# Optimization experiments

Measured on AMD Instinct MI355X. Metric: run time of the kernel, lower is better.

Reference implementation:

```python
import jax, jax.numpy as jnp
import numpy as np

B, T, DIM = 8, 2048, 512
DM, EXPAND, NSTATE, HDIM, L = 128, 2, 16, 64, 2
DINNER = DM * EXPAND            # 256
NH = DINNER // HDIM             # 4 heads
CONVDIM = DINNER + 2 * NSTATE   # 288 (n_groups=1)
PROJ = DINNER + CONVDIM + NH    # 548
K = 4                           # conv kernel (HF default)
EPS = 1e-5


def setup_inputs() -> dict:
    key = jax.random.key(0)
    ks = jax.random.split(key, 8)
    s = 0.02
    return {
        "x": jax.random.normal(ks[0], (B, T, DIM), jnp.float32),
        "in_w": jax.random.normal(ks[1], (DIM, DM), jnp.float32) * s,
        "in_b": jnp.zeros((DM,), jnp.float32),
        "norm_w": jnp.ones((L, DM), jnp.float32),
        "inproj_w": jax.random.normal(ks[2], (L, DM, PROJ), jnp.float32) * s,
        "conv_w": jax.random.normal(ks[3], (L, CONVDIM, 1, K), jnp.float32) * 0.2,
        "conv_b": jnp.zeros((L, CONVDIM), jnp.float32),
        "A_log": jnp.log(jax.random.uniform(ks[4], (L, NH), jnp.float32, 1.0, 8.0)),
        "D": jnp.ones((L, NH), jnp.float32),
        "dt_bias": jnp.log(jnp.expm1(jax.random.uniform(ks[5], (L, NH), jnp.float32, 1e-3, 0.1))),
        "gnorm_w": jnp.ones((L, DINNER), jnp.float32),
        "outproj_w": jax.random.normal(ks[6], (L, DINNER, DM), jnp.float32) * s,
        "normf_w": jnp.ones((DM,), jnp.float32),
        "out_w": jax.random.normal(ks[7], (DM, DIM), jnp.float32) * s,
        "out_b": jnp.zeros((DIM,), jnp.float32),
    }


def _rmsnorm(x, w):
    var = jnp.mean(x * x, axis=-1, keepdims=True)
    return x * jax.lax.rsqrt(var + EPS) * w


def _gated_rmsnorm(y, gate, w):
    y = y * jax.nn.silu(gate)
    var = jnp.mean(y * y, axis=-1, keepdims=True)
    return y * jax.lax.rsqrt(var + EPS) * w


def _causal_conv(h, w, b):
    # h: [B,T,C] depthwise causal conv, kernel K, left pad K-1
    out = jax.lax.conv_general_dilated(
        h.swapaxes(1, 2), w, (1,), [(K - 1, 0)],
        feature_group_count=CONVDIM,
        dimension_numbers=("NCH", "OIH", "NCH"))
    return out.swapaxes(1, 2) + b


def _ssd(xs, dt, A, Bm, Cm, Dh):
    # selective state-space scan (math-equivalent to HF Mamba2 chunked SSD)
    # xs [B,T,H,P], dt [B,T,H], A [H], Bm/Cm [B,T,N], Dh [H]
    dA = jnp.exp(dt * A)  # [B,T,H]

    def step(state, inp):
        dA_t, dt_t, x_t, B_t, C_t = inp
        dBx = dt_t[:, :, None, None] * x_t[..., None] * B_t[:, None, None, :]
        state = state * dA_t[:, :, None, None] + dBx  # [B,H,P,N]
        y = jnp.einsum("bhpn,bn->bhp", state, C_t)
        return state, y

    init = jnp.zeros((xs.shape[0], NH, HDIM, NSTATE), xs.dtype)
    _, ys = jax.lax.scan(step, init, (dA.swapaxes(0, 1), dt.swapaxes(0, 1),
                                      xs.swapaxes(0, 1), Bm.swapaxes(0, 1), Cm.swapaxes(0, 1)))
    return ys.swapaxes(0, 1) + xs * Dh[None, None, :, None]


def reference(x, in_w, in_b, norm_w, inproj_w, conv_w, conv_b, A_log, D,
              dt_bias, gnorm_w, outproj_w, normf_w, out_w, out_b):
    h = x @ in_w + in_b  # [B,T,DM]
    for l in range(L):
        res = h
        hn = _rmsnorm(h, norm_w[l])
        proj = hn @ inproj_w[l]  # [B,T,PROJ]
        gate = proj[..., :DINNER]
        hBC = proj[..., DINNER:DINNER + CONVDIM]
        dt = proj[..., DINNER + CONVDIM:]
        hBC = jax.nn.silu(_causal_conv(hBC, conv_w[l], conv_b[l]))
        xs = hBC[..., :DINNER].reshape(B, T, NH, HDIM)
        Bm = hBC[..., DINNER:DINNER + NSTATE]
        Cm = hBC[..., DINNER + NSTATE:]
        A = -jnp.exp(A_log[l])
        dt = jax.nn.softplus(dt + dt_bias[l])  # time_step_limit=(0,inf): no clamp
        y = _ssd(xs, dt, A, Bm, Cm, D[l]).reshape(B, T, DINNER)
        y = _gated_rmsnorm(y, gate, gnorm_w[l])
        h = res + y @ outproj_w[l]
    h = _rmsnorm(h, normf_w)
    pooled = h.mean(axis=1)  # mean pool over T
    return pooled @ out_w + out_b
```

## Files before the change

kernel.cpp:

```cpp
#include <hip/hip_runtime.h>
#include <math.h>

typedef unsigned short ushort_t;
typedef unsigned int uint_t;

#define B_      8
#define T_      2048
#define DIMX    512
#define DM      128
#define DINNER  256
#define NSTATE  16
#define HDIM    64
#define NH      4
#define CONVDIM 288
#define PROJ    548
#define KCONV   4
#define LLAYERS 2
#define QCH     128
#define NC      (T_/QCH)
#define EPSF    1e-5f
#define MTOK    (B_*T_)

#define OFF_H      0u
#define OFF_Z      20119552u
#define OFF_DEC    21168128u
#define OFF_PART   21168640u
#define OFF_WTIN   23396864u
#define OFF_WTINP  23429632u
#define OFF_WTOUT  23503360u
#define OFF_PROJB  23600000u
#define OFF_DTRAW  28100000u
#define OFF_YB     30600000u

__device__ __forceinline__ ushort_t f2b(float f) {
    uint_t u = __builtin_bit_cast(uint_t, f);
    return (ushort_t)((u + 0x7FFFu + ((u >> 16) & 1u)) >> 16);
}
__device__ __forceinline__ float b2f(ushort_t b) {
    uint_t u = ((uint_t)b) << 16;
    return __builtin_bit_cast(float, u);
}
__device__ __forceinline__ float blo(uint_t u) { return b2f((ushort_t)(u & 0xffffu)); }
__device__ __forceinline__ float bhi(uint_t u) { return b2f((ushort_t)(u >> 16)); }

typedef short bf8 __attribute__((ext_vector_type(8)));
typedef float f4v __attribute__((ext_vector_type(4)));

__global__ __launch_bounds__(256) void k_wt_all(
    const float* __restrict__ in_w, const float* __restrict__ inproj_w,
    const float* __restrict__ outproj_w,
    ushort_t* __restrict__ wt_in, ushort_t* __restrict__ wt_inp,
    ushort_t* __restrict__ wt_out)
{
    __shared__ float tile[64][65];
    int idx = blockIdx.x;
    const float* W; ushort_t* Wt; int K, N, k0, n0;
    if (idx < 16) {
        W = in_w; Wt = wt_in; K = 512; N = 128;
        k0 = (idx & 7) * 64; n0 = (idx >> 3) * 64;
    } else if (idx < 52) {
        int r = idx - 16; int l = r / 18; r -= l * 18;
        W = inproj_w + l * 128 * PROJ; Wt = wt_inp + l * 576 * 128; K = 128; N = PROJ;
        k0 = (r & 1) * 64; n0 = (r >> 1) * 64;
    } else {
        int r = idx - 52; int l = r / 8; r -= l * 8;
        W = outproj_w + l * 256 * 128; Wt = wt_out + l * 128 * 256; K = 256; N = 128;
        k0 = (r & 3) * 64; n0 = (r >> 2) * 64;
    }
    const int tid = threadIdx.x;
#pragma unroll
    for (int it = 0; it < 16; ++it) {
        const int e = it * 256 + tid;
        const int kk = e >> 6, nn = e & 63;
        tile[kk][nn] = (n0 + nn < N) ? W[(k0 + kk) * N + (n0 + nn)] : 0.f;
    }
    __syncthreads();
#pragma unroll
    for (int it = 0; it < 16; ++it) {
        const int e = it * 256 + tid;
        const int nn = e >> 6, kk = e & 63;
        Wt[(n0 + nn) * K + k0 + kk] = f2b(tile[kk][nn]);
    }
}

template<int KTOT, int LDC, int NGUARD, int EPI, bool ABF16>
__global__ __launch_bounds__(256) void k_gemm(
    const void* __restrict__ Ap, const ushort_t* __restrict__ Bt,
    const float* __restrict__ aux, float* __restrict__ C)
{
    __shared__ ushort_t Als[64 * 136];
    __shared__ ushort_t Bls[64 * 136];
    const int m0 = blockIdx.x * 64, n0 = blockIdx.y * 64;
    const int tid = threadIdx.x;
    const int lane = tid & 63, w = tid >> 6;
    const int wm = (w >> 1) * 32, wn = (w & 1) * 32;
    const int r16 = lane & 15, q8 = (lane >> 4) * 8;

    f4v acc[2][2];
#pragma unroll
    for (int i = 0; i < 2; ++i)
#pragma unroll
        for (int j = 0; j < 2; ++j) acc[i][j] = (f4v)0.f;

    for (int kc = 0; kc < KTOT; kc += 128) {
        if constexpr (ABF16) {
            const ushort_t* A = (const ushort_t*)Ap;
#pragma unroll
            for (int i = 0; i < 4; ++i) {
                const int e = i * 2048 + tid * 8;
                const int r = e >> 7, c = e & 127;
                *(uint4*)&Als[r * 136 + c] = *(const uint4*)&A[(m0 + r) * KTOT + kc + c];
            }
        } else {
            const float* A = (const float*)Ap;
#pragma unroll
            for (int i = 0; i < 4; ++i) {
                const int e = i * 2048 + tid * 8;
                const int r = e >> 7, c = e & 127;
                const float4 f0 = *(const float4*)&A[(m0 + r) * KTOT + kc + c];
                const float4 f1 = *(const float4*)&A[(m0 + r) * KTOT + kc + c + 4];
                uint4 pk;
                pk.x = (uint_t)f2b(f0.x) | ((uint_t)f2b(f0.y) << 16);
                pk.y = (uint_t)f2b(f0.z) | ((uint_t)f2b(f0.w) << 16);
                pk.z = (uint_t)f2b(f1.x) | ((uint_t)f2b(f1.y) << 16);
                pk.w = (uint_t)f2b(f1.z) | ((uint_t)f2b(f1.w) << 16);
                *(uint4*)&Als[r * 136 + c] = pk;
            }
        }
#pragma unroll
        for (int i = 0; i < 4; ++i) {
            const int e = i * 2048 + tid * 8;
            const int r = e >> 7, c = e & 127;
            *(uint4*)&Bls[r * 136 + c] = *(const uint4*)&Bt[(n0 + r) * KTOT + kc + c];
        }
        __syncthreads();
#pragma unroll
        for (int kk = 0; kk < 128; kk += 32) {
            const bf8 a0 = *(const bf8*)&Als[(wm + r16) * 136 + kk + q8];
            const bf8 a1 = *(const bf8*)&Als[(wm + 16 + r16) * 136 + kk + q8];
            const bf8 b0 = *(const bf8*)&Bls[(wn + r16) * 136 + kk + q8];
            const bf8 b1 = *(const bf8*)&Bls[(wn + 16 + r16) * 136 + kk + q8];
            acc[0][0] = __builtin_amdgcn_mfma_f32_16x16x32_bf16(a0, b0, acc[0][0], 0, 0, 0);
            acc[0][1] = __builtin_amdgcn_mfma_f32_16x16x32_bf16(a0, b1, acc[0][1], 0, 0, 0);
            acc[1][0] = __builtin_amdgcn_mfma_f32_16x16x32_bf16(a1, b0, acc[1][0], 0, 0, 0);
            acc[1][1] = __builtin_amdgcn_mfma_f32_16x16x32_bf16(a1, b1, acc[1][1], 0, 0, 0);
        }
        __syncthreads();
    }
    const int q4 = (lane >> 4) * 4;
#pragma unroll
    for (int i = 0; i < 2; ++i)
#pragma unroll
        for (int j = 0; j < 2; ++j)
#pragma unroll
            for (int r = 0; r < 4; ++r) {
                const int grow = m0 + wm + i * 16 + q4 + r;
                const int gcol = n0 + wn + j * 16 + r16;
                if (NGUARD == 0 || gcol < NGUARD) {
                    float v = acc[i][j][r];
                    if (EPI == 1) v += aux[gcol];
                    if (EPI == 2) v += C[grow * LDC + gcol];
                    C[grow * LDC + gcol] = v;
                }
            }
}

__global__ __launch_bounds__(256) void k_gemm_rms(
    const float* __restrict__ h, const float* __restrict__ nw,
    const ushort_t* __restrict__ Bt, ushort_t* __restrict__ projb,
    float* __restrict__ dtraw)
{
    __shared__ ushort_t Als[64 * 136];
    __shared__ ushort_t Bls[64 * 136];
    const int m0 = blockIdx.x * 64;
    const int tid = threadIdx.x;
    const int lane = tid & 63, w = tid >> 6;
    const int wm = (w >> 1) * 32, wn = (w & 1) * 32;
    const int r16 = lane & 15, q8 = (lane >> 4) * 8;
    const int q4 = (lane >> 4) * 4;

#pragma unroll
    for (int i = 0; i < 4; ++i) {
        const int e = i * 2048 + tid * 8;
        const int r = e >> 7, c = e & 127;
        const float4 f0 = *(const float4*)&h[(m0 + r) * 128 + c];
        const float4 f1 = *(const float4*)&h[(m0 + r) * 128 + c + 4];
        float ss = f0.x * f0.x + f0.y * f0.y + f0.z * f0.z + f0.w * f0.w
                 + f1.x * f1.x + f1.y * f1.y + f1.z * f1.z + f1.w * f1.w;
#pragma unroll
        for (int off = 1; off < 16; off <<= 1) ss += __shfl_xor(ss, off);
        const float rs = rsqrtf(ss * (1.f / 128.f) + EPSF);
        const float4 w0 = *(const float4*)&nw[c];
        const float4 w1 = *(const float4*)&nw[c + 4];
        uint4 pk;
        pk.x = (uint_t)f2b(f0.x * rs * w0.x) | ((uint_t)f2b(f0.y * rs * w0.y) << 16);
        pk.y = (uint_t)f2b(f0.z * rs * w0.z) | ((uint_t)f2b(f0.w * rs * w0.w) << 16);
        pk.z = (uint_t)f2b(f1.x * rs * w1.x) | ((uint_t)f2b(f1.y * rs * w1.y) << 16);
        pk.w = (uint_t)f2b(f1.z * rs * w1.z) | ((uint_t)f2b(f1.w * rs * w1.w) << 16);
        *(uint4*)&Als[r * 136 + c] = pk;
    }

#pragma unroll
    for (int half = 0; half < 2; ++half) {
        const int n0 = blockIdx.y * 128 + half * 64;
        if (n0 >= 576) break;
#pragma unroll
        for (int i = 0; i < 4; ++i) {
            const int e = i * 2048 + tid * 8;
            const int r = e >> 7, c = e & 127;
            *(uint4*)&Bls[r * 136 + c] = *(const uint4*)&Bt[(n0 + r) * 128 + c];
        }
        __syncthreads();

        f4v acc[2][2];
#pragma unroll
        for (int i = 0; i < 2; ++i)
#pragma unroll
            for (int j = 0; j < 2; ++j) acc[i][j] = (f4v)0.f;
#pragma unroll
        for (int kk = 0; kk < 128; kk += 32) {
            const bf8 a0 = *(const bf8*)&Als[(wm + r16) * 136 + kk + q8];
            const bf8 a1 = *(const bf8*)&Als[(wm + 16 + r16) * 136 + kk + q8];
            const bf8 b0 = *(const bf8*)&Bls[(wn + r16) * 136 + kk + q8];
            const bf8 b1 = *(const bf8*)&Bls[(wn + 16 + r16) * 136 + kk + q8];
            acc[0][0] = __builtin_amdgcn_mfma_f32_16x16x32_bf16(a0, b0, acc[0][0], 0, 0, 0);
            acc[0][1] = __builtin_amdgcn_mfma_f32_16x16x32_bf16(a0, b1, acc[0][1], 0, 0, 0);
            acc[1][0] = __builtin_amdgcn_mfma_f32_16x16x32_bf16(a1, b0, acc[1][0], 0, 0, 0);
            acc[1][1] = __builtin_amdgcn_mfma_f32_16x16x32_bf16(a1, b1, acc[1][1], 0, 0, 0);
        }
        __syncthreads();

#pragma unroll
        for (int i = 0; i < 2; ++i)
#pragma unroll
            for (int j = 0; j < 2; ++j)
#pragma unroll
                for (int r = 0; r < 4; ++r) {
                    const int grow = m0 + wm + i * 16 + q4 + r;
                    const int gcol = n0 + wn + j * 16 + r16;
                    if (gcol < 544) projb[grow * 544 + gcol] = f2b(acc[i][j][r]);
                    else if (gcol < PROJ) dtraw[grow * 4 + (gcol - 544)] = acc[i][j][r];
                }
    }
}

__global__ __launch_bounds__(256) void k_gemm_gn(
    const ushort_t* __restrict__ yb, const ushort_t* __restrict__ projb,
    const float* __restrict__ gw, const ushort_t* __restrict__ Bt,
    float* __restrict__ C)
{
    __shared__ ushort_t Als[64 * 264];
    __shared__ ushort_t Bls[64 * 136];
    const int m0 = blockIdx.x * 64, n0 = blockIdx.y * 64;
    const int tid = threadIdx.x;
    const int lane = tid & 63, w = tid >> 6;
    const int wm = (w >> 1) * 32, wn = (w & 1) * 32;
    const int r16 = lane & 15, q8 = (lane >> 4) * 8;

#pragma unroll
    for (int i = 0; i < 8; ++i) {
        const int e = i * 2048 + tid * 8;
        const int r = e >> 8, c = e & 255;
        const uint4 yv = *(const uint4*)&yb[(m0 + r) * 256 + c];
        const uint4 gv = *(const uint4*)&projb[(m0 + r) * 544 + c];
        const float g0 = blo(gv.x), g1 = bhi(gv.x), g2 = blo(gv.y), g3 = bhi(gv.y);
        const float g4 = blo(gv.z), g5 = bhi(gv.z), g6 = blo(gv.w), g7 = bhi(gv.w);
        float v0 = blo(yv.x) * (g0 / (1.f + __expf(-g0)));
        float v1 = bhi(yv.x) * (g1 / (1.f + __expf(-g1)));
        float v2 = blo(yv.y) * (g2 / (1.f + __expf(-g2)));
        float v3 = bhi(yv.y) * (g3 / (1.f + __expf(-g3)));
        float v4 = blo(yv.z) * (g4 / (1.f + __expf(-g4)));
        float v5 = bhi(yv.z) * (g5 / (1.f + __expf(-g5)));
        float v6 = blo(yv.w) * (g6 / (1.f + __expf(-g6)));
        float v7 = bhi(yv.w) * (g7 / (1.f + __expf(-g7)));
        float ss = v0 * v0 + v1 * v1 + v2 * v2 + v3 * v3
                 + v4 * v4 + v5 * v5 + v6 * v6 + v7 * v7;
#pragma unroll
        for (int off = 1; off < 32; off <<= 1) ss += __shfl_xor(ss, off);
        const float rs = rsqrtf(ss * (1.f / 256.f) + EPSF);
        const float4 w0 = *(const float4*)&gw[c];
        const float4 w1 = *(const float4*)&gw[c + 4];
        uint4 pk;
        pk.x = (uint_t)f2b(v0 * rs * w0.x) | ((uint_t)f2b(v1 * rs * w0.y) << 16);
        pk.y = (uint_t)f2b(v2 * rs * w0.z) | ((uint_t)f2b(v3 * rs * w0.w) << 16);
        pk.z = (uint_t)f2b(v4 * rs * w1.x) | ((uint_t)f2b(v5 * rs * w1.y) << 16);
        pk.w = (uint_t)f2b(v6 * rs * w1.z) | ((uint_t)f2b(v7 * rs * w1.w) << 16);
        *(uint4*)&Als[r * 264 + c] = pk;
    }

    f4v acc[2][2];
#pragma unroll
    for (int i = 0; i < 2; ++i)
#pragma unroll
        for (int j = 0; j < 2; ++j) acc[i][j] = (f4v)0.f;

    for (int kc = 0; kc < 256; kc += 128) {
#pragma unroll
        for (int i = 0; i < 4; ++i) {
            const int e = i * 2048 + tid * 8;
            const int r = e >> 7, c = e & 127;
            *(uint4*)&Bls[r * 136 + c] = *(const uint4*)&Bt[(n0 + r) * 256 + kc + c];
        }
        __syncthreads();
#pragma unroll
        for (int kk = 0; kk < 128; kk += 32) {
            const bf8 a0 = *(const bf8*)&Als[(wm + r16) * 264 + kc + kk + q8];
            const bf8 a1 = *(const bf8*)&Als[(wm + 16 + r16) * 264 + kc + kk + q8];
            const bf8 b0 = *(const bf8*)&Bls[(wn + r16) * 136 + kk + q8];
            const bf8 b1 = *(const bf8*)&Bls[(wn + 16 + r16) * 136 + kk + q8];
            acc[0][0] = __builtin_amdgcn_mfma_f32_16x16x32_bf16(a0, b0, acc[0][0], 0, 0, 0);
            acc[0][1] = __builtin_amdgcn_mfma_f32_16x16x32_bf16(a0, b1, acc[0][1], 0, 0, 0);
            acc[1][0] = __builtin_amdgcn_mfma_f32_16x16x32_bf16(a1, b0, acc[1][0], 0, 0, 0);
            acc[1][1] = __builtin_amdgcn_mfma_f32_16x16x32_bf16(a1, b1, acc[1][1], 0, 0, 0);
        }
        __syncthreads();
    }

    const int q4 = (lane >> 4) * 4;
#pragma unroll
    for (int i = 0; i < 2; ++i)
#pragma unroll
        for (int j = 0; j < 2; ++j)
#pragma unroll
            for (int r = 0; r < 4; ++r) {
                const int grow = m0 + wm + i * 16 + q4 + r;
                const int gcol = n0 + wn + j * 16 + r16;
                C[grow * 128 + gcol] += acc[i][j][r];
            }
}

__device__ __forceinline__ void dt_scan_wave0(
    const float* __restrict__ dtraw, const float* __restrict__ A_log,
    const float* __restrict__ dt_bias, int l, int hh, int m0, int lane,
    float* __restrict__ cumls, float* __restrict__ dtls)
{
    const float Ah = -expf(A_log[l * NH + hh]);
    const float bias = dt_bias[l * NH + hh];
    const float r0 = dtraw[(m0 + lane) * 4 + hh] + bias;
    const float r1 = dtraw[(m0 + 64 + lane) * 4 + hh] + bias;
    const float dt0 = (r0 > 20.f) ? r0 : log1pf(expf(r0));
    const float dt1 = (r1 > 20.f) ? r1 : log1pf(expf(r1));
    float v0 = dt0 * Ah, v1 = dt1 * Ah;
#pragma unroll
    for (int off = 1; off < 64; off <<= 1) {
        const int src = (lane - off) & 63;
        const float s0 = __shfl(v0, src);
        const float s1 = __shfl(v1, src);
        v0 += (lane >= off) ? s0 : 0.f;
        v1 += (lane >= off) ? s1 : s0;
    }
    v1 += v0;
    cumls[lane] = v0; cumls[64 + lane] = v1;
    dtls[lane]  = dt0; dtls[64 + lane]  = dt1;
}

__global__ __launch_bounds__(256) void k_ssd_state(
    const ushort_t* __restrict__ projb, const float* __restrict__ dtraw,
    const float* __restrict__ cw, const float* __restrict__ cb,
    const float* __restrict__ A_log, const float* __restrict__ dt_bias,
    float* __restrict__ zbuf, float* __restrict__ dec, int l)
{
    __shared__ ushort_t Xt[64 * 136];
    __shared__ ushort_t wB[16 * 136];
    __shared__ ushort_t pX[131 * 64];
    __shared__ ushort_t pB[131 * 16];
    __shared__ float cumls[QCH];
    __shared__ float dtls[QCH];
    const int bid = blockIdx.x;
    const int c = bid & (NC - 1);
    const int hh = (bid / NC) & (NH - 1);
    const int b = bid / (NC * NH);
    const int m0 = b * T_ + c * QCH;
    const int tid = threadIdx.x;
    const int lane = tid & 63;

    if (tid < 64) {
        dt_scan_wave0(dtraw, A_log, dt_bias, l, hh, m0, lane, cumls, dtls);
    } else {
        const int t0 = c * QCH;
        for (int e = tid - 64; e < 131 * 8; e += 192) {
            const int ls = e >> 3, j = e & 7;
            const int tb = t0 + ls - 3;
            uint4 v; v.x = 0u; v.y = 0u; v.z = 0u; v.w = 0u;
            if (tb >= 0) v = *(const uint4*)&projb[(b * T_ + tb) * 544 + 256 + hh * 64 + j * 8];
            *(uint4*)&pX[ls * 64 + j * 8] = v;
        }
        for (int e = tid - 64; e < 131 * 2; e += 192) {
            const int ls = e >> 1, j = e & 1;
            const int tb = t0 + ls - 3;
            uint4 v; v.x = 0u; v.y = 0u; v.z = 0u; v.w = 0u;
            if (tb >= 0) v = *(const uint4*)&projb[(b * T_ + tb) * 544 + 512 + j * 8];
            *(uint4*)&pB[ls * 16 + j * 8] = v;
        }
    }
    __syncthreads();
    const float clast = cumls[QCH - 1];

    {
        const int p = tid & 63;
        const int s0 = tid >> 6;
        const float* wp = cw + (l * CONVDIM + hh * 64 + p) * KCONV;
        const float bbv = cb[l * CONVDIM + hh * 64 + p];
#pragma unroll
        for (int pass = 0; pass < 32; ++pass) {
            const int s = pass * 4 + s0;
            float a = bbv;
#pragma unroll
            for (int k = 0; k < KCONV; ++k) a += b2f(pX[(s + k) * 64 + p]) * wp[k];
            Xt[p * 136 + s] = f2b(a / (1.f + __expf(-a)));
        }
    }
    {
        const int n = tid & 15;
        const int s0 = tid >> 4;
        const float* wp = cw + (l * CONVDIM + 256 + n) * KCONV;
        const float bbv = cb[l * CONVDIM + 256 + n];
#pragma unroll
        for (int pass = 0; pass < 8; ++pass) {
            const int s = pass * 16 + s0;
            float a = bbv;
#pragma unroll
            for (int k = 0; k < KCONV; ++k) a += b2f(pB[(s + k) * 16 + n]) * wp[k];
            const ushort_t sb = f2b(a / (1.f + __expf(-a)));
            const float w = __expf(clast - cumls[s]) * dtls[s];
            wB[n * 136 + s] = f2b(w * b2f(sb));
        }
    }
    __syncthreads();

    const int w = tid >> 6;
    const int r16 = lane & 15, q8 = (lane >> 4) * 8, q4 = (lane >> 4) * 4;
    f4v acc = (f4v)0.f;
#pragma unroll
    for (int kc = 0; kc < 128; kc += 32) {
        const bf8 a = *(const bf8*)&Xt[(w * 16 + r16) * 136 + kc + q8];
        const bf8 bb = *(const bf8*)&wB[r16 * 136 + kc + q8];
        acc = __builtin_amdgcn_mfma_f32_16x16x32_bf16(a, bb, acc, 0, 0, 0);
    }
#pragma unroll
    for (int r = 0; r < 4; ++r) {
        const int p = w * 16 + q4 + r;
        zbuf[bid * 1024 + p * 16 + r16] = acc[r];
    }
    if (tid == 0) dec[bid] = __expf(clast);
}

__global__ __launch_bounds__(256) void k_ssd_y(
    const ushort_t* __restrict__ projb, const float* __restrict__ dtraw,
    const float* __restrict__ cw, const float* __restrict__ cb,
    const float* __restrict__ A_log, const float* __restrict__ dt_bias,
    const float* __restrict__ zbuf, const float* __restrict__ dec,
    const float* __restrict__ Dvec, ushort_t* __restrict__ yb, int l)
{
    __shared__ ushort_t Xt[64 * 136];
    __shared__ ushort_t BlsT[128 * 40];
    __shared__ ushort_t ClsT[128 * 40];
    __shared__ ushort_t Gls[128 * 136];
    __shared__ ushort_t Spt[64 * 40];
    __shared__ float cumls[QCH];
    __shared__ float dtls[QCH];
    ushort_t* pX = Gls;
    ushort_t* pB = Gls + 131 * 64;
    ushort_t* pC = Gls + 131 * 64 + 131 * 16;
    const int bid = blockIdx.x;
    const int c = bid & (NC - 1);
    const int hh = (bid / NC) & (NH - 1);
    const int b = bid / (NC * NH);
    const int bh = bid >> 4;
    const int m0 = b * T_ + c * QCH;
    const int tid = threadIdx.x;
    const int lane = tid & 63;

    if (tid < 64) {
        dt_scan_wave0(dtraw, A_log, dt_bias, l, hh, m0, lane, cumls, dtls);
    } else {
        const int t0 = c * QCH;
        for (int e = tid - 64; e < 131 * 8; e += 192) {
            const int ls = e >> 3, j = e & 7;
            const int tb = t0 + ls - 3;
            uint4 v; v.x = 0u; v.y = 0u; v.z = 0u; v.w = 0u;
            if (tb >= 0) v = *(const uint4*)&projb[(b * T_ + tb) * 544 + 256 + hh * 64 + j * 8];
            *(uint4*)&pX[ls * 64 + j * 8] = v;
        }
        for (int e = tid - 64; e < 131 * 2; e += 192) {
            const int ls = e >> 1, j = e & 1;
            const int tb = t0 + ls - 3;
            uint4 v0; v0.x = 0u; v0.y = 0u; v0.z = 0u; v0.w = 0u;
            uint4 v1 = v0;
            if (tb >= 0) {
                v0 = *(const uint4*)&projb[(b * T_ + tb) * 544 + 512 + j * 8];
                v1 = *(const uint4*)&projb[(b * T_ + tb) * 544 + 528 + j * 8];
            }
            *(uint4*)&pB[ls * 16 + j * 8] = v0;
            *(uint4*)&pC[ls * 16 + j * 8] = v1;
        }
    }
    __syncthreads();

    {
        const int p = tid & 63;
        const int s0 = tid >> 6;
        const float* wp = cw + (l * CONVDIM + hh * 64 + p) * KCONV;
        const float bbv = cb[l * CONVDIM + hh * 64 + p];
#pragma unroll
        for (int pass = 0; pass < 32; ++pass) {
            const int s = pass * 4 + s0;
            float a = bbv;
#pragma unroll
            for (int k = 0; k < KCONV; ++k) a += b2f(pX[(s + k) * 64 + p]) * wp[k];
            Xt[p * 136 + s] = f2b(a / (1.f + __expf(-a)));
        }
    }
    {
        const int n = tid & 15;
        const int s0 = tid >> 4;
        const float* wpB = cw + (l * CONVDIM + 256 + n) * KCONV;
        const float bbB = cb[l * CONVDIM + 256 + n];
        const float* wpC = cw + (l * CONVDIM + 272 + n) * KCONV;
        const float bbC = cb[l * CONVDIM + 272 + n];
#pragma unroll
        for (int pass = 0; pass < 8; ++pass) {
            const int s = pass * 16 + s0;
            float aB = bbB, aC = bbC;
#pragma unroll
            for (int k = 0; k < KCONV; ++k) {
                aB += b2f(pB[(s + k) * 16 + n]) * wpB[k];
                aC += b2f(pC[(s + k) * 16 + n]) * wpC[k];
            }
            BlsT[s * 40 + n] = f2b(aB / (1.f + __expf(-aB)));
            ClsT[s * 40 + n] = f2b(aC / (1.f + __expf(-aC)));
            BlsT[s * 40 + 16 + n] = 0;
            ClsT[s * 40 + 16 + n] = 0;
        }
    }
    {
        float4 S; S.x = 0.f; S.y = 0.f; S.z = 0.f; S.w = 0.f;
        for (int cc = 0; cc < c; ++cc) {
            const float d = dec[bh * NC + cc];
            const float4 z = *(const float4*)(zbuf + (bh * NC + cc) * 1024 + tid * 4);
            S.x = S.x * d + z.x; S.y = S.y * d + z.y;
            S.z = S.z * d + z.z; S.w = S.w * d + z.w;
        }
        const int p = tid >> 2, n = (tid & 3) * 4;
        Spt[p * 40 + n]     = f2b(S.x);
        Spt[p * 40 + n + 1] = f2b(S.y);
        Spt[p * 40 + n + 2] = f2b(S.z);
        Spt[p * 40 + n + 3] = f2b(S.w);
        Spt[p * 40 + 16 + n]     = 0;
        Spt[p * 40 + 16 + n + 1] = 0;
        Spt[p * 40 + 16 + n + 2] = 0;
        Spt[p * 40 + 16 + n + 3] = 0;
    }
    __syncthreads();

    const int w = tid >> 6;
    const int wrow = w * 32;
    const int r16 = lane & 15, q8 = (lane >> 4) * 8, q4 = (lane >> 4) * 4;
    const float Dh = Dvec[l * NH + hh];

    bf8 cfr[2];
#pragma unroll
    for (int i = 0; i < 2; ++i)
        cfr[i] = *(const bf8*)&ClsT[(wrow + i * 16 + r16) * 40 + q8];

    float cumt[8], et[8];
#pragma unroll
    for (int i = 0; i < 2; ++i)
#pragma unroll
        for (int r = 0; r < 4; ++r) {
            const int t = wrow + i * 16 + q4 + r;
            cumt[i * 4 + r] = cumls[t];
            et[i * 4 + r] = __expf(cumls[t]);
        }

    f4v acc[2][4];
#pragma unroll
    for (int j = 0; j < 4; ++j) {
        const bf8 sf = *(const bf8*)&Spt[(j * 16 + r16) * 40 + q8];
#pragma unroll
        for (int i = 0; i < 2; ++i) {
            f4v z = (f4v)0.f;
            z = __builtin_amdgcn_mfma_f32_16x16x32_bf16(cfr[i], sf, z, 0, 0, 0);
#pragma unroll
            for (int r = 0; r < 4; ++r) {
                const int t = wrow + i * 16 + q4 + r;
                const int p = j * 16 + r16;
                acc[i][j][r] = z[r] * et[i * 4 + r] + Dh * b2f(Xt[p * 136 + t]);
            }
        }
    }

#pragma unroll
    for (int ts = 0; ts < 8; ++ts) {
        const bf8 bf = *(const bf8*)&BlsT[(ts * 16 + r16) * 40 + q8];
        const int s = ts * 16 + r16;
        const float cs = cumls[s];
        const float ds = dtls[s];
#pragma unroll
        for (int i = 0; i < 2; ++i) {
            f4v g = (f4v)0.f;
            g = __builtin_amdgcn_mfma_f32_16x16x32_bf16(cfr[i], bf, g, 0, 0, 0);
#pragma unroll
            for (int r = 0; r < 4; ++r) {
                const int t = wrow + i * 16 + q4 + r;
                const float val = (s <= t) ? __expf(cumt[i * 4 + r] - cs) * ds * g[r] : 0.f;
                Gls[t * 136 + s] = f2b(val);
            }
        }
    }
    __syncthreads();

#pragma unroll
    for (int kc = 0; kc < 128; kc += 32) {
        bf8 af[2];
#pragma unroll
        for (int i = 0; i < 2; ++i)
            af[i] = *(const bf8*)&Gls[(wrow + i * 16 + r16) * 136 + kc + q8];
#pragma unroll
        for (int j = 0; j < 4; ++j) {
            const bf8 xf = *(const bf8*)&Xt[(j * 16 + r16) * 136 + kc + q8];
#pragma unroll
            for (int i = 0; i < 2; ++i)
                acc[i][j] = __builtin_amdgcn_mfma_f32_16x16x32_bf16(af[i], xf, acc[i][j], 0, 0, 0);
        }
    }

#pragma unroll
    for (int i = 0; i < 2; ++i)
#pragma unroll
        for (int r = 0; r < 4; ++r) {
            const int t = wrow + i * 16 + q4 + r;
#pragma unroll
            for (int j = 0; j < 4; ++j) {
                const int p = j * 16 + r16;
                yb[(m0 + t) * DINNER + hh * 64 + p] = f2b(acc[i][j][r]);
            }
        }
}

__global__ __launch_bounds__(256) void k_finalnorm_pool(
    const float* __restrict__ h, const float* __restrict__ nfw,
    float* __restrict__ part)
{
    __shared__ float ht[2048];
    __shared__ float red[256];
    __shared__ float rstd[16];
    __shared__ float padd[256];
    const int tile = blockIdx.x & 127;
    const int b = blockIdx.x >> 7;
    const int m0 = b * T_ + tile * 16;
    const int tid = threadIdx.x;
    for (int e = tid; e < 2048; e += 256) ht[e] = h[m0 * DM + e];
    __syncthreads();
    {
        const int tg = tid >> 4, j0 = tid & 15;
        float p = 0.f;
#pragma unroll
        for (int k = 0; k < 8; ++k) { const float v = ht[tg * 128 + j0 + 16 * k]; p += v * v; }
        red[tid] = p;
    }
    __syncthreads();
    if (tid < 16) {
        float s = 0.f;
#pragma unroll
        for (int q = 0; q < 16; ++q) s += red[tid * 16 + q];
        rstd[tid] = rsqrtf(s * (1.f / 128.f) + EPSF);
    }
    __syncthreads();
    const int d = tid & 127, half = tid >> 7;
    float ps = 0.f;
#pragma unroll
    for (int i0 = 0; i0 < 8; ++i0) { const int i = half + 2 * i0; ps += ht[i * 128 + d] * rstd[i]; }
    padd[tid] = ps;
    __syncthreads();
    if (tid < 128) part[(b * 128 + tile) * 128 + tid] = (padd[tid] + padd[128 + tid]) * nfw[tid];
}

__global__ __launch_bounds__(256) void k_head(
    const float* __restrict__ part, const float* __restrict__ ow,
    const float* __restrict__ ob, float* __restrict__ out)
{
    __shared__ float pooled[128];
    const int b = blockIdx.x;
    const int tid = threadIdx.x;
    if (tid < 128) {
        float s = 0.f;
        for (int tile = 0; tile < 128; ++tile) s += part[(b * 128 + tile) * 128 + tid];
        pooled[tid] = s * (1.f / (float)T_);
    }
    __syncthreads();
    for (int o = tid; o < DIMX; o += 256) {
        float acc = ob[o];
#pragma unroll 4
        for (int d = 0; d < 128; ++d) acc += pooled[d] * ow[d * DIMX + o];
        out[b * DIMX + o] = acc;
    }
}

extern "C" void kernel_launch(void* const* d_in, const int* in_sizes, int n_in,
                              void* d_out, int out_size, void* d_ws, size_t ws_size,
                              hipStream_t stream)
{
    const float* x         = (const float*)d_in[0];
    const float* in_w      = (const float*)d_in[1];
    const float* in_b      = (const float*)d_in[2];
    const float* norm_w    = (const float*)d_in[3];
    const float* inproj_w  = (const float*)d_in[4];
    const float* conv_w    = (const float*)d_in[5];
    const float* conv_b    = (const float*)d_in[6];
    const float* A_log     = (const float*)d_in[7];
    const float* Dvec      = (const float*)d_in[8];
    const float* dt_bias   = (const float*)d_in[9];
    const float* gnorm_w   = (const float*)d_in[10];
    const float* outproj_w = (const float*)d_in[11];
    const float* normf_w   = (const float*)d_in[12];
    const float* out_w     = (const float*)d_in[13];
    const float* out_b     = (const float*)d_in[14];

    float* ws    = (float*)d_ws;
    float* h     = ws + OFF_H;
    float* zbuf  = ws + OFF_Z;
    float* dec   = ws + OFF_DEC;
    float* part  = ws + OFF_PART;
    float* dtraw = ws + OFF_DTRAW;
    ushort_t* projb = (ushort_t*)(ws + OFF_PROJB);
    ushort_t* yb    = (ushort_t*)(ws + OFF_YB);
    ushort_t* wt_in  = (ushort_t*)(ws + OFF_WTIN);
    ushort_t* wt_inp = (ushort_t*)(ws + OFF_WTINP);
    ushort_t* wt_out = (ushort_t*)(ws + OFF_WTOUT);

    k_wt_all<<<68, 256, 0, stream>>>(in_w, inproj_w, outproj_w, wt_in, wt_inp, wt_out);

    k_gemm<512, 128, 0, 1, false><<<dim3(MTOK / 64, 2), 256, 0, stream>>>(x, wt_in, in_b, h);

    for (int l = 0; l < LLAYERS; ++l) {
        k_gemm_rms<<<dim3(MTOK / 64, 5), 256, 0, stream>>>(
            h, norm_w + l * DM, wt_inp + l * 576 * 128, projb, dtraw);
        k_ssd_state<<<B_ * NH * NC, 256, 0, stream>>>(
            projb, dtraw, conv_w, conv_b, A_log, dt_bias, zbuf, dec, l);
        k_ssd_y<<<B_ * NH * NC, 256, 0, stream>>>(
            projb, dtraw, conv_w, conv_b, A_log, dt_bias, zbuf, dec, Dvec, yb, l);
        k_gemm_gn<<<dim3(MTOK / 64, 2), 256, 0, stream>>>(
            yb, projb, gnorm_w + l * DINNER, wt_out + l * 128 * 256, h);
    }

    k_finalnorm_pool<<<B_ * (T_ / 16), 256, 0, stream>>>(h, normf_w, part);
    k_head<<<B_, 256, 0, stream>>>(part, out_w, out_b, (float*)d_out);
}
```

Before: 250.7 us.

## Cover full N per block in input and output GEMMs, skip last-chunk state

The input projection GEMM and the gated-norm output GEMM now have each block compute all 128 output columns, launching half as many blocks. The A tile (fp32→bf16 conversion, or the gated RMSNorm of y) is computed once per row tile instead of twice. The SSD state kernel also returns early for the last chunk of each sequence, whose carried-out state is never consumed. The trade-off is fewer blocks (256) for roughly 256 CUs and longer serial work per block. The input GEMM also keeps twice as many accumulators live.

```diff
diff --git a/kernel.cpp b/kernel.cpp
--- a/kernel.cpp
+++ b/kernel.cpp
@@ -83,86 +83,77 @@
     }
 }
 
-template<int KTOT, int LDC, int NGUARD, int EPI, bool ABF16>
-__global__ __launch_bounds__(256) void k_gemm(
-    const void* __restrict__ Ap, const ushort_t* __restrict__ Bt,
-    const float* __restrict__ aux, float* __restrict__ C)
+__global__ __launch_bounds__(256) void k_gemm_in(
+    const float* __restrict__ x, const ushort_t* __restrict__ Bt,
+    const float* __restrict__ ib, float* __restrict__ C)
 {
     __shared__ ushort_t Als[64 * 136];
     __shared__ ushort_t Bls[64 * 136];
-    const int m0 = blockIdx.x * 64, n0 = blockIdx.y * 64;
+    const int m0 = blockIdx.x * 64;
     const int tid = threadIdx.x;
     const int lane = tid & 63, w = tid >> 6;
     const int wm = (w >> 1) * 32, wn = (w & 1) * 32;
     const int r16 = lane & 15, q8 = (lane >> 4) * 8;
 
-    f4v acc[2][2];
-#pragma unroll
-    for (int i = 0; i < 2; ++i)
-#pragma unroll
-        for (int j = 0; j < 2; ++j) acc[i][j] = (f4v)0.f;
-
-    for (int kc = 0; kc < KTOT; kc += 128) {
-        if constexpr (ABF16) {
-            const ushort_t* A = (const ushort_t*)Ap;
+    f4v acc[2][2][2];
+#pragma unroll
+    for (int hf = 0; hf < 2; ++hf)
+#pragma unroll
+        for (int i = 0; i < 2; ++i)
+#pragma unroll
+            for (int j = 0; j < 2; ++j) acc[hf][i][j] = (f4v)0.f;
+
+    for (int kc = 0; kc < 512; kc += 128) {
+#pragma unroll
+        for (int i = 0; i < 4; ++i) {
+            const int e = i * 2048 + tid * 8;
+            const int r = e >> 7, c = e & 127;
+            const float4 f0 = *(const float4*)&x[(m0 + r) * 512 + kc + c];
+            const float4 f1 = *(const float4*)&x[(m0 + r) * 512 + kc + c + 4];
+            uint4 pk;
+            pk.x = (uint_t)f2b(f0.x) | ((uint_t)f2b(f0.y) << 16);
+            pk.y = (uint_t)f2b(f0.z) | ((uint_t)f2b(f0.w) << 16);
+            pk.z = (uint_t)f2b(f1.x) | ((uint_t)f2b(f1.y) << 16);
+            pk.w = (uint_t)f2b(f1.z) | ((uint_t)f2b(f1.w) << 16);
+            *(uint4*)&Als[r * 136 + c] = pk;
+        }
+#pragma unroll
+        for (int hf = 0; hf < 2; ++hf) {
+            const int n0 = hf * 64;
 #pragma unroll
             for (int i = 0; i < 4; ++i) {
                 const int e = i * 2048 + tid * 8;
                 const int r = e >> 7, c = e & 127;
-                *(uint4*)&Als[r * 136 + c] = *(const uint4*)&A[(m0 + r) * KTOT + kc + c];
-            }
-        } else {
-            const float* A = (const float*)Ap;
-#pragma unroll
-            for (int i = 0; i < 4; ++i) {
-                const int e = i * 2048 + tid * 8;
-                const int r = e >> 7, c = e & 127;
-                const float4 f0 = *(const float4*)&A[(m0 + r) * KTOT + kc + c];
-                const float4 f1 = *(const float4*)&A[(m0 + r) * KTOT + kc + c + 4];
-                uint4 pk;
-                pk.x = (uint_t)f2b(f0.x) | ((uint_t)f2b(f0.y) << 16);
-                pk.y = (uint_t)f2b(f0.z) | ((uint_t)f2b(f0.w) << 16);
-                pk.z = (uint_t)f2b(f1.x) | ((uint_t)f2b(f1.y) << 16);
-                pk.w = (uint_t)f2b(f1.z) | ((uint_t)f2b(f1.w) << 16);
-                *(uint4*)&Als[r * 136 + c] = pk;
-            }
-        }
-#pragma unroll
-        for (int i = 0; i < 4; ++i) {
-            const int e = i * 2048 + tid * 8;
-            const int r = e >> 7, c = e & 127;
-            *(uint4*)&Bls[r * 136 + c] = *(const uint4*)&Bt[(n0 + r) * KTOT + kc + c];
-        }
-        __syncthreads();
-#pragma unroll
-        for (int kk = 0; kk < 128; kk += 32) {
-            const bf8 a0 = *(const bf8*)&Als[(wm + r16) * 136 + kk + q8];
-            const bf8 a1 = *(const bf8*)&Als[(wm + 16 + r16) * 136 + kk + q8];
-            const bf8 b0 = *(const bf8*)&Bls[(wn + r16) * 136 + kk + q8];
-            const bf8 b1 = *(const bf8*)&Bls[(wn + 16 + r16) * 136 + kk + q8];
-            acc[0][0] = __builtin_amdgcn_mfma_f32_16x16x32_bf16(a0, b0, acc[0][0], 0, 0, 0);
-            acc[0][1] = __builtin_amdgcn_mfma_f32_16x16x32_bf16(a0, b1, acc[0][1], 0, 0, 0);
-            acc[1][0] = __builtin_amdgcn_mfma_f32_16x16x32_bf16(a1, b0, acc[1][0], 0, 0, 0);
-            acc[1][1] = __builtin_amdgcn_mfma_f32_16x16x32_bf16(a1, b1, acc[1][1], 0, 0, 0);
-        }
-        __syncthreads();
+                *(uint4*)&Bls[r * 136 + c] = *(const uint4*)&Bt[(n0 + r) * 512 + kc + c];
+            }
+            __syncthreads();
+#pragma unroll
+            for (int kk = 0; kk < 128; kk += 32) {
+                const bf8 a0 = *(const bf8*)&Als[(wm + r16) * 136 + kk + q8];
+                const bf8 a1 = *(const bf8*)&Als[(wm + 16 + r16) * 136 + kk + q8];
+                const bf8 b0 = *(const bf8*)&Bls[(wn + r16) * 136 + kk + q8];
+                const bf8 b1 = *(const bf8*)&Bls[(wn + 16 + r16) * 136 + kk + q8];
+                acc[hf][0][0] = __builtin_amdgcn_mfma_f32_16x16x32_bf16(a0, b0, acc[hf][0][0], 0, 0, 0);
+                acc[hf][0][1] = __builtin_amdgcn_mfma_f32_16x16x32_bf16(a0, b1, acc[hf][0][1], 0, 0, 0);
+                acc[hf][1][0] = __builtin_amdgcn_mfma_f32_16x16x32_bf16(a1, b0, acc[hf][1][0], 0, 0, 0);
+                acc[hf][1][1] = __builtin_amdgcn_mfma_f32_16x16x32_bf16(a1, b1, acc[hf][1][1], 0, 0, 0);
+            }
+            __syncthreads();
+        }
     }
     const int q4 = (lane >> 4) * 4;
 #pragma unroll
-    for (int i = 0; i < 2; ++i)
-#pragma unroll
-        for (int j = 0; j < 2; ++j)
-#pragma unroll
-            for (int r = 0; r < 4; ++r) {
-                const int grow = m0 + wm + i * 16 + q4 + r;
-                const int gcol = n0 + wn + j * 16 + r16;
-                if (NGUARD == 0 || gcol < NGUARD) {
-                    float v = acc[i][j][r];
-                    if (EPI == 1) v += aux[gcol];
-                    if (EPI == 2) v += C[grow * LDC + gcol];
-                    C[grow * LDC + gcol] = v;
+    for (int hf = 0; hf < 2; ++hf)
+#pragma unroll
+        for (int i = 0; i < 2; ++i)
+#pragma unroll
+            for (int j = 0; j < 2; ++j)
+#pragma unroll
+                for (int r = 0; r < 4; ++r) {
+                    const int grow = m0 + wm + i * 16 + q4 + r;
+                    const int gcol = hf * 64 + wn + j * 16 + r16;
+                    C[grow * 128 + gcol] = acc[hf][i][j][r] + ib[gcol];
                 }
-            }
 }
 
 __global__ __launch_bounds__(256) void k_gemm_rms(
@@ -251,11 +242,12 @@
 {
     __shared__ ushort_t Als[64 * 264];
     __shared__ ushort_t Bls[64 * 136];
-    const int m0 = blockIdx.x * 64, n0 = blockIdx.y * 64;
+    const int m0 = blockIdx.x * 64;
     const int tid = threadIdx.x;
     const int lane = tid & 63, w = tid >> 6;
     const int wm = (w >> 1) * 32, wn = (w & 1) * 32;
     const int r16 = lane & 15, q8 = (lane >> 4) * 8;
+    const int q4 = (lane >> 4) * 4;
 
 #pragma unroll
     for (int i = 0; i < 8; ++i) {
@@ -288,45 +280,48 @@
         *(uint4*)&Als[r * 264 + c] = pk;
     }
 
-    f4v acc[2][2];
-#pragma unroll
-    for (int i = 0; i < 2; ++i)
-#pragma unroll
-        for (int j = 0; j < 2; ++j) acc[i][j] = (f4v)0.f;
-
-    for (int kc = 0; kc < 256; kc += 128) {
-#pragma unroll
-        for (int i = 0; i < 4; ++i) {
-            const int e = i * 2048 + tid * 8;
-            const int r = e >> 7, c = e & 127;
-            *(uint4*)&Bls[r * 136 + c] = *(const uint4*)&Bt[(n0 + r) * 256 + kc + c];
-        }
-        __syncthreads();
-#pragma unroll
-        for (int kk = 0; kk < 128; kk += 32) {
-            const bf8 a0 = *(const bf8*)&Als[(wm + r16) * 264 + kc + kk + q8];
-            const bf8 a1 = *(const bf8*)&Als[(wm + 16 + r16) * 264 + kc + kk + q8];
-            const bf8 b0 = *(const bf8*)&Bls[(wn + r16) * 136 + kk + q8];
-            const bf8 b1 = *(const bf8*)&Bls[(wn + 16 + r16) * 136 + kk + q8];
-            acc[0][0] = __builtin_amdgcn_mfma_f32_16x16x32_bf16(a0, b0, acc[0][0], 0, 0, 0);
-            acc[0][1] = __builtin_amdgcn_mfma_f32_16x16x32_bf16(a0, b1, acc[0][1], 0, 0, 0);
-            acc[1][0] = __builtin_amdgcn_mfma_f32_16x16x32_bf16(a1, b0, acc[1][0], 0, 0, 0);
-            acc[1][1] = __builtin_amdgcn_mfma_f32_16x16x32_bf16(a1, b1, acc[1][1], 0, 0, 0);
-        }
-        __syncthreads();
-    }
-
-    const int q4 = (lane >> 4) * 4;
-#pragma unroll
-    for (int i = 0; i < 2; ++i)
-#pragma unroll
-        for (int j = 0; j < 2; ++j)
-#pragma unroll
-            for (int r = 0; r < 4; ++r) {
-                const int grow = m0 + wm + i * 16 + q4 + r;
-                const int gcol = n0 + wn + j * 16 + r16;
-                C[grow * 128 + gcol] += acc[i][j][r];
-            }
+#pragma unroll
+    for (int half = 0; half < 2; ++half) {
+        const int n0 = half * 64;
+        f4v acc[2][2];
+#pragma unroll
+        for (int i = 0; i < 2; ++i)
+#pragma unroll
+            for (int j = 0; j < 2; ++j) acc[i][j] = (f4v)0.f;
+
+        for (int kc = 0; kc < 256; kc += 128) {
+#pragma unroll
+            for (int i = 0; i < 4; ++i) {
+                const int e = i * 2048 + tid * 8;
+                const int r = e >> 7, c = e & 127;
+                *(uint4*)&Bls[r * 136 + c] = *(const uint4*)&Bt[(n0 + r) * 256 + kc + c];
+            }
+            __syncthreads();
+#pragma unroll
+            for (int kk = 0; kk < 128; kk += 32) {
+                const bf8 a0 = *(const bf8*)&Als[(wm + r16) * 264 + kc + kk + q8];
+                const bf8 a1 = *(const bf8*)&Als[(wm + 16 + r16) * 264 + kc + kk + q8];
+                const bf8 b0 = *(const bf8*)&Bls[(wn + r16) * 136 + kk + q8];
+                const bf8 b1 = *(const bf8*)&Bls[(wn + 16 + r16) * 136 + kk + q8];
+                acc[0][0] = __builtin_amdgcn_mfma_f32_16x16x32_bf16(a0, b0, acc[0][0], 0, 0, 0);
+                acc[0][1] = __builtin_amdgcn_mfma_f32_16x16x32_bf16(a0, b1, acc[0][1], 0, 0, 0);
+                acc[1][0] = __builtin_amdgcn_mfma_f32_16x16x32_bf16(a1, b0, acc[1][0], 0, 0, 0);
+                acc[1][1] = __builtin_amdgcn_mfma_f32_16x16x32_bf16(a1, b1, acc[1][1], 0, 0, 0);
+            }
+            __syncthreads();
+        }
+
+#pragma unroll
+        for (int i = 0; i < 2; ++i)
+#pragma unroll
+            for (int j = 0; j < 2; ++j)
+#pragma unroll
+                for (int r = 0; r < 4; ++r) {
+                    const int grow = m0 + wm + i * 16 + q4 + r;
+                    const int gcol = n0 + wn + j * 16 + r16;
+                    C[grow * 128 + gcol] += acc[i][j][r];
+                }
+    }
 }
 
 __device__ __forceinline__ void dt_scan_wave0(
@@ -368,6 +363,7 @@
     __shared__ float dtls[QCH];
     const int bid = blockIdx.x;
     const int c = bid & (NC - 1);
+    if (c == NC - 1) return;
     const int hh = (bid / NC) & (NH - 1);
     const int b = bid / (NC * NH);
     const int m0 = b * T_ + c * QCH;
@@ -731,7 +727,7 @@
 
     k_wt_all<<<68, 256, 0, stream>>>(in_w, inproj_w, outproj_w, wt_in, wt_inp, wt_out);
 
-    k_gemm<512, 128, 0, 1, false><<<dim3(MTOK / 64, 2), 256, 0, stream>>>(x, wt_in, in_b, h);
+    k_gemm_in<<<MTOK / 64, 256, 0, stream>>>(x, wt_in, in_b, h);
 
     for (int l = 0; l < LLAYERS; ++l) {
         k_gemm_rms<<<dim3(MTOK / 64, 5), 256, 0, stream>>>(
@@ -740,7 +736,7 @@
             projb, dtraw, conv_w, conv_b, A_log, dt_bias, zbuf, dec, l);
         k_ssd_y<<<B_ * NH * NC, 256, 0, stream>>>(
             projb, dtraw, conv_w, conv_b, A_log, dt_bias, zbuf, dec, Dvec, yb, l);
-        k_gemm_gn<<<dim3(MTOK / 64, 2), 256, 0, stream>>>(
+        k_gemm_gn<<<MTOK / 64, 256, 0, stream>>>(
             yb, projb, gnorm_w + l * DINNER, wt_out + l * 128 * 256, h);
     }
 
```

Result: no change. 246.4 us (median of 2 runs) (-1.7%).
